# Kernel tuning notes

Hardware: AMD Instinct MI355X
Metric: run time of the kernel (lower is better)

## Reference

```python
import jax, jax.numpy as jnp
import numpy as np

H = 1024
N_HEADS = 8
HEAD_DIM = H // N_HEADS
META_DIM = 256
VOCAB = 32000
MIN_W, MAX_W = 0.1, 5.0
LN_EPS = 1e-5


def _ln(x, g, b):
    mu = jnp.mean(x, axis=-1, keepdims=True)
    var = jnp.var(x, axis=-1, keepdims=True)
    return (x - mu) * jax.lax.rsqrt(var + LN_EPS) * g + b


def setup_inputs() -> dict:
    key = jax.random.key(0)
    ks = jax.random.split(key, 16)
    B, S = 4, 2048
    s = 0.02
    return {
        "hidden_states": jax.random.normal(ks[0], (B, S, H), jnp.float32),
        "token_ids": jax.random.randint(ks[1], (B, S), 0, VOCAB, jnp.int32),
        "attention_mask": jnp.ones((B, S), jnp.bool_),
        "pos_embed": jax.random.normal(ks[2], (1, S, H), jnp.float32),
        # torch nn.MultiheadAttention params
        "in_proj_w": jax.random.normal(ks[3], (3 * H, H), jnp.float32) * s,
        "in_proj_b": jnp.zeros((3 * H,), jnp.float32),
        "out_w": jax.random.normal(ks[4], (H, H), jnp.float32) * s,
        "out_b": jnp.zeros((H,), jnp.float32),
        # meta_network params (torch Linear convention: y = x @ W.T + b)
        "w1": jax.random.normal(ks[5], (META_DIM, 2 * H), jnp.float32) * s,
        "b1": jnp.zeros((META_DIM,), jnp.float32),
        "g1": jnp.ones((META_DIM,), jnp.float32),
        "beta1": jnp.zeros((META_DIM,), jnp.float32),
        "w2": jax.random.normal(ks[6], (META_DIM // 2, META_DIM), jnp.float32) * s,
        "b2": jnp.zeros((META_DIM // 2,), jnp.float32),
        "g2": jnp.ones((META_DIM // 2,), jnp.float32),
        "beta2": jnp.zeros((META_DIM // 2,), jnp.float32),
        "w3": jax.random.normal(ks[7], (1, META_DIM // 2), jnp.float32) * s,
        "b3": jnp.zeros((1,), jnp.float32),
        # tensorized ImportanceMemory.get_importance: one scalar per vocab id
        "importance_table": jax.random.uniform(ks[8], (VOCAB,), jnp.float32) * 0.1,
    }


def reference(hidden_states, token_ids, attention_mask, pos_embed,
              in_proj_w, in_proj_b, out_w, out_b,
              w1, b1, g1, beta1, w2, b2, g2, beta2, w3, b3,
              importance_table):
    B, S, _ = hidden_states.shape
    x = hidden_states + pos_embed[:, :S, :]

    # MultiheadAttention (batch_first, eval mode -> no dropout)
    qkv = x @ in_proj_w.T + in_proj_b                      # [B,S,3H]
    q, k, v = jnp.split(qkv, 3, axis=-1)
    q = q.reshape(B, S, N_HEADS, HEAD_DIM)
    k = k.reshape(B, S, N_HEADS, HEAD_DIM)
    v = v.reshape(B, S, N_HEADS, HEAD_DIM)
    scores = jnp.einsum('bqhd,bkhd->bhqk', q, k) / jnp.sqrt(jnp.float32(HEAD_DIM))
    scores = jnp.where(attention_mask[:, None, None, :], scores, jnp.float32(-1e9))
    attn = jax.nn.softmax(scores, axis=-1)
    ctx = jnp.einsum('bhqk,bkhd->bqhd', attn, v).reshape(B, S, H)
    attended = ctx @ out_w.T + out_b

    combined = jnp.concatenate([x, attended], axis=-1)     # [B,S,2H]
    h = jax.nn.relu(_ln(combined @ w1.T + b1, g1, beta1))
    h = jax.nn.relu(_ln(h @ w2.T + b2, g2, beta2))
    base_weights = (h @ w3.T + b3).squeeze(-1)             # [B,S]

    # tensorized per-token importance lookup + clamp (manual_weights empty)
    importance = importance_table[token_ids]               # gather [B,S]
    weight = jnp.clip(base_weights * (1.0 + importance), MIN_W, MAX_W)
    return jnp.where(attention_mask, weight, 0.0)
```

## Files before the change

kernel.cpp:

```cpp
#include <hip/hip_runtime.h>
#include <hip/hip_bf16.h>
#include <math.h>

typedef __bf16 bf16;
typedef bf16 bf16x8 __attribute__((ext_vector_type(8)));
typedef bf16 bf16x4 __attribute__((ext_vector_type(4)));
typedef float f32x4 __attribute__((ext_vector_type(4)));

#define HDIM 1024
#define NHEADS 8
#define HD 128
#define MD1 256
#define MD2 128
#define LNEPS 1e-5f

__device__ __forceinline__ f32x4 mfma16(bf16x8 a, bf16x8 b, f32x4 c) {
  return __builtin_amdgcn_mfma_f32_16x16x32_bf16(a, b, c, 0, 0, 0);
}

__device__ __forceinline__ void gload_lds16(const bf16* g, bf16* l) {
  __builtin_amdgcn_global_load_lds(
      (const __attribute__((address_space(1))) void*)g,
      (__attribute__((address_space(3))) void*)l, 16, 0, 0);
}

__global__ void k_prep_all(
    const float* __restrict__ hs, const float* __restrict__ pos,
    bf16* __restrict__ xbf, int SH, int nprep,
    const float* __restrict__ s0, bf16* __restrict__ d0, int n0,
    const float* __restrict__ s1, bf16* __restrict__ d1, int n1,
    const float* __restrict__ s2, bf16* __restrict__ d2, int n2,
    const float* __restrict__ s3, bf16* __restrict__ d3, int n3) {
  int i = (blockIdx.x * blockDim.x + threadIdx.x) * 4;
  if (i < nprep) {
    float4 a = *(const float4*)(hs + i);
    float4 p = *(const float4*)(pos + (i % SH));
    bf16x4 o;
    o[0] = (bf16)(a.x + p.x); o[1] = (bf16)(a.y + p.y);
    o[2] = (bf16)(a.z + p.z); o[3] = (bf16)(a.w + p.w);
    *(bf16x4*)(xbf + i) = o;
    return;
  }
  int j = i - nprep;
  const float* s; bf16* d;
  if (j < n0)                { s = s0 + j; d = d0 + j; }
  else if (j < n0 + n1)      { s = s1 + (j - n0); d = d1 + (j - n0); }
  else if (j < n0 + n1 + n2) { s = s2 + (j - n0 - n1); d = d2 + (j - n0 - n1); }
  else                       { s = s3 + (j - n0 - n1 - n2); d = d3 + (j - n0 - n1 - n2); }
  float4 v = *(const float4*)s;
  bf16x4 o;
  o[0] = (bf16)v.x; o[1] = (bf16)v.y; o[2] = (bf16)v.z; o[3] = (bf16)v.w;
  *(bf16x4*)d = o;
}

__global__ void k_b1p(const float* __restrict__ w1, const float* __restrict__ ob,
                      const float* __restrict__ b1, float* __restrict__ b1p) {
  const int t = threadIdx.x;
  const int n = blockIdx.x * 64 + (t >> 2);
  const int jq = t & 3;
  const float* row = w1 + (size_t)n * 2048 + 1024 + jq * 256;
  const float* obp = ob + jq * 256;
  float acc = 0.f;
  for (int j = 0; j < 256; j += 4) {
    float4 a = *(const float4*)(row + j);
    float4 o = *(const float4*)(obp + j);
    acc += a.x * o.x + a.y * o.y + a.z * o.z + a.w * o.w;
  }
  acc += __shfl_xor(acc, 1);
  acc += __shfl_xor(acc, 2);
  if (jq == 0) b1p[n] = b1[n] + acc;
}

__global__ __launch_bounds__(256) void k_wprime(
    const bf16* __restrict__ w1full, const bf16* __restrict__ ow,
    bf16* __restrict__ Wp) {
  __shared__ bf16 Bst[64][40];
  const int tid = threadIdx.x;
  const int w = tid >> 6, lane = tid & 63;
  const int quad = lane >> 4, l16 = lane & 15;
  const int d0 = blockIdx.x * 64, n0 = blockIdx.y * 64;
  const bf16* arow = w1full + (size_t)(n0 + w * 16 + l16) * 2048 + 1024;
  f32x4 acc[4] = {};
  for (int k0 = 0; k0 < 1024; k0 += 32) {
    const int kk = tid >> 3, dd8 = (tid & 7) * 8;
    bf16x8 v = *(const bf16x8*)(ow + (size_t)(k0 + kk) * 1024 + d0 + dd8);
    __syncthreads();
#pragma unroll
    for (int jj = 0; jj < 8; ++jj) Bst[dd8 + jj][kk] = v[jj];
    __syncthreads();
    bf16x8 af = *(const bf16x8*)(arow + k0 + quad * 8);
#pragma unroll
    for (int dg = 0; dg < 4; ++dg) {
      bf16x8 bfr = *(const bf16x8*)&Bst[dg * 16 + l16][quad * 8];
      acc[dg] = mfma16(af, bfr, acc[dg]);
    }
  }
#pragma unroll
  for (int dg = 0; dg < 4; ++dg) {
    const int d = d0 + dg * 16 + l16;
#pragma unroll
    for (int i = 0; i < 4; ++i)
      Wp[(size_t)(n0 + w * 16 + quad * 4 + i) * 1024 + d] = (bf16)acc[dg][i];
  }
}

__global__ __launch_bounds__(256) void k_gemm_qkv(
    const bf16* __restrict__ A, const bf16* __restrict__ Bw,
    const float* __restrict__ bias, bf16* __restrict__ Qo,
    bf16* __restrict__ Ko, bf16* __restrict__ VTo, int S, int K) {
  __shared__ bf16 As[128 * 64];
  __shared__ bf16 Bs[128 * 64];
  const int tid = threadIdx.x;
  const int w = tid >> 6, lane = tid & 63;
  const int quad = lane >> 4, l16 = lane & 15;
  const int wm = w & 1, wn = w >> 1;
  const int tm = blockIdx.x * 128, tn = blockIdx.y * 128;

  const int tq = tid >> 3, t8 = tid & 7;
  const bf16 *ap[4], *bp[4];
#pragma unroll
  for (int c = 0; c < 4; ++c) {
    const int r = c * 32 + tq;
    const int col = ((t8 ^ ((r ^ (r >> 3)) & 7)) * 8);
    ap[c] = A + (size_t)(tm + r) * K + col;
    bp[c] = Bw + (size_t)(tn + r) * K + col;
  }
  bf16* lA = As + (size_t)tid * 8;
  bf16* lB = Bs + (size_t)tid * 8;

  int fam[4], fbn[4], ram[4], rbn[4];
#pragma unroll
  for (int mt = 0; mt < 4; ++mt) {
    const int r = wm * 64 + mt * 16 + l16;
    ram[mt] = r; fam[mt] = (r ^ (r >> 3)) & 7;
    const int r2 = wn * 64 + mt * 16 + l16;
    rbn[mt] = r2; fbn[mt] = (r2 ^ (r2 >> 3)) & 7;
  }

  f32x4 acc[4][4] = {};
  for (int k0 = 0; k0 < K; k0 += 64) {
#pragma unroll
    for (int c = 0; c < 4; ++c) {
      gload_lds16(ap[c] + k0, lA + c * 2048);
      gload_lds16(bp[c] + k0, lB + c * 2048);
    }
    __syncthreads();
#pragma unroll
    for (int ks = 0; ks < 2; ++ks) {
      bf16x8 af[4], bfr[4];
#pragma unroll
      for (int mt = 0; mt < 4; ++mt)
        af[mt] = *(const bf16x8*)&As[ram[mt] * 64 + (((ks * 4 + quad) ^ fam[mt]) << 3)];
#pragma unroll
      for (int nt = 0; nt < 4; ++nt)
        bfr[nt] = *(const bf16x8*)&Bs[rbn[nt] * 64 + (((ks * 4 + quad) ^ fbn[nt]) << 3)];
#pragma unroll
      for (int mt = 0; mt < 4; ++mt)
#pragma unroll
        for (int nt = 0; nt < 4; ++nt)
          acc[mt][nt] = mfma16(af[mt], bfr[nt], acc[mt][nt]);
    }
    __syncthreads();
  }

  const int region = tn >> 10;
  const int btile = tm / S, s0 = tm % S;
#pragma unroll
  for (int nt = 0; nt < 4; ++nt) {
    const int col = tn + wn * 64 + nt * 16 + l16;
    const float bv = bias[col];
#pragma unroll
    for (int mt = 0; mt < 4; ++mt) {
      if (region == 2) {
        const int d = col - 2048, hh = d >> 7, dd = d & 127;
        const int sb = s0 + wm * 64 + mt * 16 + quad * 4;
        bf16x4 o4;
#pragma unroll
        for (int i = 0; i < 4; ++i) o4[i] = (bf16)(acc[mt][nt][i] + bv);
        *(bf16x4*)&VTo[((size_t)(btile * NHEADS + hh) * HD + dd) * S + sb] = o4;
      } else {
        bf16* dst = (region == 0) ? Qo : Ko;
        const int cc = (region == 0) ? col : col - 1024;
#pragma unroll
        for (int i = 0; i < 4; ++i) {
          const int row = tm + wm * 64 + mt * 16 + quad * 4 + i;
          dst[(size_t)row * HDIM + cc] = (bf16)(acc[mt][nt][i] + bv);
        }
      }
    }
  }
}

__global__ __launch_bounds__(256) void k_flash(
    const bf16* __restrict__ Qg, const bf16* __restrict__ Kg,
    const bf16* __restrict__ VTg, const int* __restrict__ mask,
    bf16* __restrict__ ctx, int S) {
  __shared__ bf16 Ks[64][136];
  __shared__ bf16 Vt[128 * 64];
  __shared__ bf16 Ps[8 * 1024];
  __shared__ float biass[64];
  const int tid = threadIdx.x, w = tid >> 6, lane = tid & 63;
  const int quad = lane >> 4, l16 = lane & 15;
  const int bh = blockIdx.y, b = bh / NHEADS, h = bh % NHEADS;
  const int q0 = blockIdx.x * 128 + w * 32;
  const size_t bS = (size_t)b * S;
  const bf16* Qb = Qg + bS * HDIM + h * HD;
  const bf16* Kb = Kg + bS * HDIM + h * HD;
  const bf16* Vb = VTg + (size_t)bh * HD * S;
  const int* mrow = mask + bS;

  bf16x8 qf[2][4];
#pragma unroll
  for (int qt = 0; qt < 2; ++qt)
#pragma unroll
    for (int s = 0; s < 4; ++s)
      qf[qt][s] = *(const bf16x8*)(Qb + (size_t)(q0 + qt * 16 + l16) * HDIM + s * 32 + quad * 8);

  float lsum[2] = {0.f, 0.f};
  f32x4 o[2][8] = {};
  const float scale2 = 0.08838834764831845f * 1.4426950408889634f;

  const int nchunk = S / 64;
  bf16x8 kreg[4], vreg[4];
  int mreg = (tid < 64) ? mrow[tid] : 0;
#pragma unroll
  for (int it = 0; it < 4; ++it) {
    const int cid = tid + it * 256;
    kreg[it] = *(const bf16x8*)(Kb + (size_t)(cid >> 4) * HDIM + (cid & 15) * 8);
    vreg[it] = *(const bf16x8*)(Vb + (size_t)(cid >> 3) * S + (cid & 7) * 8);
  }

  for (int c0 = 0; c0 < nchunk; ++c0) {
    __syncthreads();
#pragma unroll
    for (int it = 0; it < 4; ++it) {
      const int cid = tid + it * 256;
      *(bf16x8*)&Ks[cid >> 4][(cid & 15) * 8] = kreg[it];
      const int vd = cid >> 3, vkb = cid & 7;
      *(bf16x8*)&Vt[vd * 64 + ((vkb ^ (vd & 7)) << 3)] = vreg[it];
    }
    if (tid < 64) biass[tid] = mreg ? 0.f : -1e9f;
    __syncthreads();
    const int key0n = ((c0 + 1 < nchunk) ? c0 + 1 : c0) * 64;
    if (tid < 64) mreg = mrow[key0n + tid];
#pragma unroll
    for (int it = 0; it < 4; ++it) {
      const int cid = tid + it * 256;
      kreg[it] = *(const bf16x8*)(Kb + (size_t)(key0n + (cid >> 4)) * HDIM + (cid & 15) * 8);
      vreg[it] = *(const bf16x8*)(Vb + (size_t)(cid >> 3) * S + key0n + (cid & 7) * 8);
    }
    f32x4 s4[2][4] = {};
#pragma unroll
    for (int g = 0; g < 4; ++g)
#pragma unroll
      for (int s = 0; s < 4; ++s) {
        bf16x8 kf = *(const bf16x8*)&Ks[g * 16 + l16][s * 32 + quad * 8];
        s4[0][g] = mfma16(kf, qf[0][s], s4[0][g]);
        s4[1][g] = mfma16(kf, qf[1][s], s4[1][g]);
      }
#pragma unroll
    for (int qt = 0; qt < 2; ++qt) {
      const int base = (w * 2 + qt) * 1024;
#pragma unroll
      for (int g = 0; g < 4; ++g) {
        bf16x4 pk;
#pragma unroll
        for (int i = 0; i < 4; ++i) {
          const float p = exp2f(fmaf(s4[qt][g][i], scale2, biass[g * 16 + quad * 4 + i]));
          lsum[qt] += p;
          pk[i] = (bf16)p;
        }
        const int sw = (2 * g + (quad >> 1)) ^ (l16 & 7);
        *(bf16x4*)&Ps[base + l16 * 64 + sw * 8 + (quad & 1) * 4] = pk;
      }
    }
#pragma unroll
    for (int kk = 0; kk < 2; ++kk) {
      const int kb = kk * 4 + quad;
      bf16x8 pf0 = *(const bf16x8*)&Ps[(w * 2) * 1024 + l16 * 64 + ((kb ^ (l16 & 7)) << 3)];
      bf16x8 pf1 = *(const bf16x8*)&Ps[(w * 2 + 1) * 1024 + l16 * 64 + ((kb ^ (l16 & 7)) << 3)];
#pragma unroll
      for (int dg = 0; dg < 8; ++dg) {
        const int d = dg * 16 + l16;
        bf16x8 vf = *(const bf16x8*)&Vt[d * 64 + ((kb ^ (d & 7)) << 3)];
        o[0][dg] = mfma16(pf0, vf, o[0][dg]);
        o[1][dg] = mfma16(pf1, vf, o[1][dg]);
      }
    }
  }

#pragma unroll
  for (int qt = 0; qt < 2; ++qt) {
    lsum[qt] += __shfl_xor(lsum[qt], 16);
    lsum[qt] += __shfl_xor(lsum[qt], 32);
  }
#pragma unroll
  for (int qt = 0; qt < 2; ++qt)
#pragma unroll
    for (int i = 0; i < 4; ++i) {
      const float ls = __shfl(lsum[qt], quad * 4 + i);
      const float inv = 1.0f / ls;
      const int row = q0 + qt * 16 + quad * 4 + i;
#pragma unroll
      for (int dg = 0; dg < 8; ++dg)
        ctx[(bS + row) * HDIM + h * HD + dg * 16 + l16] = (bf16)(o[qt][dg][i] * inv);
    }
}

__global__ __launch_bounds__(256) void k_meta12(
    const bf16* __restrict__ A1, const bf16* __restrict__ A2,
    const bf16* __restrict__ Bw1, const bf16* __restrict__ Wp,
    const float* __restrict__ b1p, const float* __restrict__ g1,
    const float* __restrict__ be1,
    const bf16* __restrict__ Bw2, const float* __restrict__ b2,
    const float* __restrict__ g2, const float* __restrict__ be2,
    const float* __restrict__ w3, const float* __restrict__ b3,
    const int* __restrict__ tok, const int* __restrict__ msk,
    const float* __restrict__ imp, float* __restrict__ out) {
  __shared__ char smem[44032];
  __shared__ float part_s[64][4];
  __shared__ float part_q[64][4];
  bf16 (*As)[40]  = (bf16(*)[40])smem;
  bf16 (*Bs)[40]  = (bf16(*)[40])(smem + 5120);
  bf16 (*h1s)[264] = (bf16(*)[264])smem;
  bf16 (*Bs2)[40] = (bf16(*)[40])(smem + 33792);
  const int tid = threadIdx.x;
  const int w = tid >> 6, lane = tid & 63;
  const int quad = lane >> 4, l16 = lane & 15;
  const int tm = blockIdx.x * 64;
  const int lr = tid >> 2, lc = (tid & 3) * 8;

  f32x4 acc[4][4] = {};
  for (int k0 = 0; k0 < 2048; k0 += 32) {
    const int kg = k0 + lc;
    const bf16* ap = (kg < 1024) ? (A1 + (size_t)(tm + lr) * 1024 + kg)
                                 : (A2 + (size_t)(tm + lr) * 1024 + (kg - 1024));
    *(bf16x8*)&As[lr][lc] = *(const bf16x8*)ap;
#pragma unroll
    for (int it = 0; it < 4; ++it) {
      const int row = lr + it * 64;
      const bf16* bp = (kg < 1024) ? (Bw1 + (size_t)row * 2048 + kg)
                                   : (Wp + (size_t)row * 1024 + (kg - 1024));
      *(bf16x8*)&Bs[row][lc] = *(const bf16x8*)bp;
    }
    __syncthreads();
    bf16x8 af[4], bfr[4];
#pragma unroll
    for (int mt = 0; mt < 4; ++mt) af[mt] = *(const bf16x8*)&As[mt * 16 + l16][quad * 8];
#pragma unroll
    for (int nt = 0; nt < 4; ++nt)
      bfr[nt] = *(const bf16x8*)&Bs[w * 64 + nt * 16 + l16][quad * 8];
#pragma unroll
    for (int mt = 0; mt < 4; ++mt)
#pragma unroll
      for (int nt = 0; nt < 4; ++nt)
        acc[mt][nt] = mfma16(af[mt], bfr[nt], acc[mt][nt]);
    __syncthreads();
  }

  float bv[4], gv[4], bev[4];
#pragma unroll
  for (int nt = 0; nt < 4; ++nt) {
    const int col = w * 64 + nt * 16 + l16;
    bv[nt] = b1p[col]; gv[nt] = g1[col]; bev[nt] = be1[col];
  }
#pragma unroll
  for (int mt = 0; mt < 4; ++mt)
#pragma unroll
    for (int i = 0; i < 4; ++i) {
      float s = 0.f, q = 0.f;
#pragma unroll
      for (int nt = 0; nt < 4; ++nt) {
        const float v = acc[mt][nt][i] + bv[nt];
        s += v; q += v * v;
      }
#pragma unroll
      for (int off = 1; off < 16; off <<= 1) { s += __shfl_xor(s, off); q += __shfl_xor(q, off); }
      if (l16 == 0) {
        const int row = mt * 16 + quad * 4 + i;
        part_s[row][w] = s; part_q[row][w] = q;
      }
    }
  __syncthreads();
#pragma unroll
  for (int mt = 0; mt < 4; ++mt)
#pragma unroll
    for (int i = 0; i < 4; ++i) {
      const int row = mt * 16 + quad * 4 + i;
      const float4 ps = *(const float4*)part_s[row];
      const float4 pq = *(const float4*)part_q[row];
      const float sum = ps.x + ps.y + ps.z + ps.w;
      const float sq = pq.x + pq.y + pq.z + pq.w;
      const float mean = sum / MD1;
      const float var = sq / MD1 - mean * mean;
      const float r = rsqrtf(var + LNEPS);
#pragma unroll
      for (int nt = 0; nt < 4; ++nt) {
        const int col = w * 64 + nt * 16 + l16;
        const float v = acc[mt][nt][i] + bv[nt];
        const float t = (v - mean) * r * gv[nt] + bev[nt];
        h1s[row][col] = (bf16)fmaxf(t, 0.f);
      }
    }
  __syncthreads();

  f32x4 acc2[8] = {};
  for (int k0 = 0; k0 < MD1; k0 += 32) {
    const int kg = k0 + lc;
#pragma unroll
    for (int it = 0; it < 2; ++it)
      *(bf16x8*)&Bs2[lr + it * 64][lc] =
          *(const bf16x8*)(Bw2 + (size_t)(lr + it * 64) * MD1 + kg);
    __syncthreads();
    bf16x8 af = *(const bf16x8*)&h1s[w * 16 + l16][k0 + quad * 8];
#pragma unroll
    for (int nt = 0; nt < 8; ++nt) {
      bf16x8 bfr = *(const bf16x8*)&Bs2[nt * 16 + l16][quad * 8];
      acc2[nt] = mfma16(af, bfr, acc2[nt]);
    }
    __syncthreads();
  }

  float bv2[8], gv2[8], bev2[8], w3v[8];
#pragma unroll
  for (int nt = 0; nt < 8; ++nt) {
    const int col = nt * 16 + l16;
    bv2[nt] = b2[col]; gv2[nt] = g2[col]; bev2[nt] = be2[col]; w3v[nt] = w3[col];
  }
  const float b3v = b3[0];
#pragma unroll
  for (int i = 0; i < 4; ++i) {
    float s = 0.f, q = 0.f;
#pragma unroll
    for (int nt = 0; nt < 8; ++nt) {
      const float v = acc2[nt][i] + bv2[nt];
      s += v; q += v * v;
    }
#pragma unroll
    for (int off = 1; off < 16; off <<= 1) { s += __shfl_xor(s, off); q += __shfl_xor(q, off); }
    const float mean = s / MD2;
    const float var = q / MD2 - mean * mean;
    const float r = rsqrtf(var + LNEPS);
    float d = 0.f;
#pragma unroll
    for (int nt = 0; nt < 8; ++nt) {
      const float v = acc2[nt][i] + bv2[nt];
      const float t = (v - mean) * r * gv2[nt] + bev2[nt];
      d += fmaxf(t, 0.f) * w3v[nt];
    }
#pragma unroll
    for (int off = 1; off < 16; off <<= 1) d += __shfl_xor(d, off);
    if (l16 == 0) {
      const int row = tm + w * 16 + quad * 4 + i;
      float wt = (d + b3v) * (1.f + imp[tok[row]]);
      wt = fminf(fmaxf(wt, 0.1f), 5.0f);
      out[row] = msk[row] ? wt : 0.f;
    }
  }
}

extern "C" void kernel_launch(void* const* d_in, const int* in_sizes, int n_in,
                              void* d_out, int out_size, void* d_ws, size_t ws_size,
                              hipStream_t stream) {
  const float* hs  = (const float*)d_in[0];
  const int*   tok = (const int*)d_in[1];
  const int*   msk = (const int*)d_in[2];
  const float* pos = (const float*)d_in[3];
  const float* inw = (const float*)d_in[4];
  const float* inb = (const float*)d_in[5];
  const float* ow  = (const float*)d_in[6];
  const float* ob  = (const float*)d_in[7];
  const float* w1  = (const float*)d_in[8];
  const float* b1  = (const float*)d_in[9];
  const float* g1  = (const float*)d_in[10];
  const float* be1 = (const float*)d_in[11];
  const float* w2  = (const float*)d_in[12];
  const float* b2  = (const float*)d_in[13];
  const float* g2  = (const float*)d_in[14];
  const float* be2 = (const float*)d_in[15];
  const float* w3  = (const float*)d_in[16];
  const float* b3  = (const float*)d_in[17];
  const float* imp = (const float*)d_in[18];

  const int SH = in_sizes[3];
  const int S  = SH / HDIM;
  const int Bsz = in_sizes[0] / SH;
  const int M = Bsz * S;

  char* ws = (char*)d_ws;
  const size_t MB2 = (size_t)M * HDIM * 2;
  size_t off = 0;
  bf16* xbf = (bf16*)(ws + off);  off += MB2;
  bf16* Qb  = (bf16*)(ws + off);  off += MB2;
  bf16* Kb  = (bf16*)(ws + off);  off += MB2;
  bf16* VTb = (bf16*)(ws + off);  off += MB2;
  bf16* ctx = (bf16*)(ws + off);  off += MB2;
  bf16* winp = (bf16*)(ws + off); off += (size_t)3 * HDIM * HDIM * 2;
  bf16* wout = (bf16*)(ws + off); off += (size_t)HDIM * HDIM * 2;
  bf16* w1b = (bf16*)(ws + off);  off += (size_t)MD1 * 2 * HDIM * 2;
  bf16* w2b = (bf16*)(ws + off);  off += (size_t)MD2 * MD1 * 2;
  bf16* Wp  = (bf16*)(ws + off);  off += (size_t)MD1 * HDIM * 2;
  float* b1p = (float*)(ws + off); off += (size_t)MD1 * 4;

  const int nprep = M * HDIM;
  const int n0 = 3 * HDIM * HDIM, n1 = HDIM * HDIM, n2 = MD1 * 2 * HDIM, n3 = MD2 * MD1;
  k_prep_all<<<(nprep + n0 + n1 + n2 + n3) / 4 / 256, 256, 0, stream>>>(
      hs, pos, xbf, SH, nprep, inw, winp, n0, ow, wout, n1, w1, w1b, n2, w2, w2b, n3);
  k_b1p<<<MD1 / 64, 256, 0, stream>>>(w1, ob, b1, b1p);
  k_wprime<<<dim3(HDIM / 64, MD1 / 64), 256, 0, stream>>>(w1b, wout, Wp);
  k_gemm_qkv<<<dim3(M / 128, (3 * HDIM) / 128), 256, 0, stream>>>(
      xbf, winp, inb, Qb, Kb, VTb, S, HDIM);
  k_flash<<<dim3(S / 128, Bsz * NHEADS), 256, 0, stream>>>(Qb, Kb, VTb, msk, ctx, S);
  k_meta12<<<M / 64, 256, 0, stream>>>(xbf, ctx, w1b, Wp, b1p, g1, be1,
                                       w2b, b2, g2, be2, w3, b3, tok, msk, imp,
                                       (float*)d_out);
}
```

Baseline: 382.7 us.

## Fuse weight-prep kernels and switch flash attention to direct global-to-LDS loads

Merges the conversion, W' product and bias-fold kernels into one launch by block-index dispatch. The W' product now reads fp32 weights directly, so the bf16 out-projection copy is no longer written. The flash kernel now loads K and V tiles with global_load_lds into XOR-swizzled LDS instead of staging them through registers, and remaps the 1-D grid so blocks that share a head run near each other. This lowers launch count and register pressure, but the prefetch overlap is lost because loads are issued and waited on within the same iteration, and the grid remap hardcodes the shape (8 heads × 4 batches, 16 q-blocks).

```diff
diff --git a/kernel.cpp b/kernel.cpp
--- a/kernel.cpp
+++ b/kernel.cpp
@@ -24,42 +24,82 @@
       (__attribute__((address_space(3))) void*)l, 16, 0, 0);
 }
 
-__global__ void k_prep_all(
+__global__ __launch_bounds__(256) void k_prep_all(
     const float* __restrict__ hs, const float* __restrict__ pos,
     bf16* __restrict__ xbf, int SH, int nprep,
-    const float* __restrict__ s0, bf16* __restrict__ d0, int n0,
-    const float* __restrict__ s1, bf16* __restrict__ d1, int n1,
-    const float* __restrict__ s2, bf16* __restrict__ d2, int n2,
-    const float* __restrict__ s3, bf16* __restrict__ d3, int n3) {
-  int i = (blockIdx.x * blockDim.x + threadIdx.x) * 4;
-  if (i < nprep) {
-    float4 a = *(const float4*)(hs + i);
-    float4 p = *(const float4*)(pos + (i % SH));
+    const float* __restrict__ inwf, bf16* __restrict__ winp, int n0,
+    const float* __restrict__ w1f, bf16* __restrict__ w1b, int n2,
+    const float* __restrict__ w2f, bf16* __restrict__ w2b, int n3,
+    const float* __restrict__ owf, const float* __restrict__ obf,
+    const float* __restrict__ b1f, bf16* __restrict__ Wp,
+    float* __restrict__ b1p, int blocks_el) {
+  const int bid = blockIdx.x;
+  const int tid = threadIdx.x;
+  if (bid < blocks_el) {
+    int i = (bid * 256 + tid) * 4;
+    if (i < nprep) {
+      float4 a = *(const float4*)(hs + i);
+      float4 p = *(const float4*)(pos + (i % SH));
+      bf16x4 o;
+      o[0] = (bf16)(a.x + p.x); o[1] = (bf16)(a.y + p.y);
+      o[2] = (bf16)(a.z + p.z); o[3] = (bf16)(a.w + p.w);
+      *(bf16x4*)(xbf + i) = o;
+      return;
+    }
+    int j = i - nprep;
+    const float* s; bf16* d;
+    if (j < n0)           { s = inwf + j; d = winp + j; }
+    else if (j < n0 + n2) { s = w1f + (j - n0); d = w1b + (j - n0); }
+    else                  { s = w2f + (j - n0 - n2); d = w2b + (j - n0 - n2); }
+    float4 v = *(const float4*)s;
     bf16x4 o;
-    o[0] = (bf16)(a.x + p.x); o[1] = (bf16)(a.y + p.y);
-    o[2] = (bf16)(a.z + p.z); o[3] = (bf16)(a.w + p.w);
-    *(bf16x4*)(xbf + i) = o;
+    o[0] = (bf16)v.x; o[1] = (bf16)v.y; o[2] = (bf16)v.z; o[3] = (bf16)v.w;
+    *(bf16x4*)d = o;
     return;
   }
-  int j = i - nprep;
-  const float* s; bf16* d;
-  if (j < n0)                { s = s0 + j; d = d0 + j; }
-  else if (j < n0 + n1)      { s = s1 + (j - n0); d = d1 + (j - n0); }
-  else if (j < n0 + n1 + n2) { s = s2 + (j - n0 - n1); d = d2 + (j - n0 - n1); }
-  else                       { s = s3 + (j - n0 - n1 - n2); d = d3 + (j - n0 - n1 - n2); }
-  float4 v = *(const float4*)s;
-  bf16x4 o;
-  o[0] = (bf16)v.x; o[1] = (bf16)v.y; o[2] = (bf16)v.z; o[3] = (bf16)v.w;
-  *(bf16x4*)d = o;
-}
-
-__global__ void k_b1p(const float* __restrict__ w1, const float* __restrict__ ob,
-                      const float* __restrict__ b1, float* __restrict__ b1p) {
-  const int t = threadIdx.x;
-  const int n = blockIdx.x * 64 + (t >> 2);
-  const int jq = t & 3;
-  const float* row = w1 + (size_t)n * 2048 + 1024 + jq * 256;
-  const float* obp = ob + jq * 256;
+  if (bid < blocks_el + 64) {
+    __shared__ bf16 Bst[64][42];
+    const int bid2 = bid - blocks_el;
+    const int d0 = (bid2 & 15) * 64, n0w = (bid2 >> 4) * 64;
+    const int w = tid >> 6, lane = tid & 63;
+    const int quad = lane >> 4, l16 = lane & 15;
+    const float* arow = w1f + (size_t)(n0w + w * 16 + l16) * 2048 + 1024;
+    f32x4 acc[4] = {};
+    for (int k0 = 0; k0 < 1024; k0 += 32) {
+      const int kk = tid >> 3, dd8 = (tid & 7) * 8;
+      float4 va = *(const float4*)(owf + (size_t)(k0 + kk) * 1024 + d0 + dd8);
+      float4 vb = *(const float4*)(owf + (size_t)(k0 + kk) * 1024 + d0 + dd8 + 4);
+      __syncthreads();
+      Bst[dd8 + 0][kk] = (bf16)va.x; Bst[dd8 + 1][kk] = (bf16)va.y;
+      Bst[dd8 + 2][kk] = (bf16)va.z; Bst[dd8 + 3][kk] = (bf16)va.w;
+      Bst[dd8 + 4][kk] = (bf16)vb.x; Bst[dd8 + 5][kk] = (bf16)vb.y;
+      Bst[dd8 + 6][kk] = (bf16)vb.z; Bst[dd8 + 7][kk] = (bf16)vb.w;
+      __syncthreads();
+      float4 fa = *(const float4*)(arow + k0 + quad * 8);
+      float4 fb = *(const float4*)(arow + k0 + quad * 8 + 4);
+      bf16x8 af;
+      af[0] = (bf16)fa.x; af[1] = (bf16)fa.y; af[2] = (bf16)fa.z; af[3] = (bf16)fa.w;
+      af[4] = (bf16)fb.x; af[5] = (bf16)fb.y; af[6] = (bf16)fb.z; af[7] = (bf16)fb.w;
+#pragma unroll
+      for (int dg = 0; dg < 4; ++dg) {
+        bf16x8 bfr = *(const bf16x8*)&Bst[dg * 16 + l16][quad * 8];
+        acc[dg] = mfma16(af, bfr, acc[dg]);
+      }
+    }
+#pragma unroll
+    for (int dg = 0; dg < 4; ++dg) {
+      const int d = d0 + dg * 16 + l16;
+#pragma unroll
+      for (int i = 0; i < 4; ++i)
+        Wp[(size_t)(n0w + w * 16 + quad * 4 + i) * 1024 + d] = (bf16)acc[dg][i];
+    }
+    return;
+  }
+  const int bid3 = bid - blocks_el - 64;
+  const int n = bid3 * 64 + (tid >> 2);
+  const int jq = tid & 3;
+  const float* row = w1f + (size_t)n * 2048 + 1024 + jq * 256;
+  const float* obp = obf + jq * 256;
   float acc = 0.f;
   for (int j = 0; j < 256; j += 4) {
     float4 a = *(const float4*)(row + j);
@@ -68,40 +108,7 @@
   }
   acc += __shfl_xor(acc, 1);
   acc += __shfl_xor(acc, 2);
-  if (jq == 0) b1p[n] = b1[n] + acc;
-}
-
-__global__ __launch_bounds__(256) void k_wprime(
-    const bf16* __restrict__ w1full, const bf16* __restrict__ ow,
-    bf16* __restrict__ Wp) {
-  __shared__ bf16 Bst[64][40];
-  const int tid = threadIdx.x;
-  const int w = tid >> 6, lane = tid & 63;
-  const int quad = lane >> 4, l16 = lane & 15;
-  const int d0 = blockIdx.x * 64, n0 = blockIdx.y * 64;
-  const bf16* arow = w1full + (size_t)(n0 + w * 16 + l16) * 2048 + 1024;
-  f32x4 acc[4] = {};
-  for (int k0 = 0; k0 < 1024; k0 += 32) {
-    const int kk = tid >> 3, dd8 = (tid & 7) * 8;
-    bf16x8 v = *(const bf16x8*)(ow + (size_t)(k0 + kk) * 1024 + d0 + dd8);
-    __syncthreads();
-#pragma unroll
-    for (int jj = 0; jj < 8; ++jj) Bst[dd8 + jj][kk] = v[jj];
-    __syncthreads();
-    bf16x8 af = *(const bf16x8*)(arow + k0 + quad * 8);
-#pragma unroll
-    for (int dg = 0; dg < 4; ++dg) {
-      bf16x8 bfr = *(const bf16x8*)&Bst[dg * 16 + l16][quad * 8];
-      acc[dg] = mfma16(af, bfr, acc[dg]);
-    }
-  }
-#pragma unroll
-  for (int dg = 0; dg < 4; ++dg) {
-    const int d = d0 + dg * 16 + l16;
-#pragma unroll
-    for (int i = 0; i < 4; ++i)
-      Wp[(size_t)(n0 + w * 16 + quad * 4 + i) * 1024 + d] = (bf16)acc[dg][i];
-  }
+  if (jq == 0) b1p[n] = b1f[n] + acc;
 }
 
 __global__ __launch_bounds__(256) void k_gemm_qkv(
@@ -195,20 +202,36 @@
     const bf16* __restrict__ Qg, const bf16* __restrict__ Kg,
     const bf16* __restrict__ VTg, const int* __restrict__ mask,
     bf16* __restrict__ ctx, int S) {
-  __shared__ bf16 Ks[64][136];
+  __shared__ bf16 Ks[64 * 128];
   __shared__ bf16 Vt[128 * 64];
   __shared__ bf16 Ps[8 * 1024];
   __shared__ float biass[64];
   const int tid = threadIdx.x, w = tid >> 6, lane = tid & 63;
   const int quad = lane >> 4, l16 = lane & 15;
-  const int bh = blockIdx.y, b = bh / NHEADS, h = bh % NHEADS;
-  const int q0 = blockIdx.x * 128 + w * 32;
+  const int p = blockIdx.x;
+  const int bh = (p & 7) * 4 + ((p >> 3) >> 4);
+  const int qb = (p >> 3) & 15;
+  const int b = bh / NHEADS, h = bh % NHEADS;
+  const int q0 = qb * 128 + w * 32;
   const size_t bS = (size_t)b * S;
   const bf16* Qb = Qg + bS * HDIM + h * HD;
   const bf16* Kb = Kg + bS * HDIM + h * HD;
   const bf16* Vb = VTg + (size_t)bh * HD * S;
   const int* mrow = mask + bS;
 
+  const bf16 *ksrc[4], *vsrc[4];
+#pragma unroll
+  for (int it = 0; it < 4; ++it) {
+    const int key = it * 16 + (tid >> 4);
+    const int g = tid & 15;
+    const int fk = (key ^ (key >> 3)) & 7;
+    const int db = (g & 8) | ((g ^ fk) & 7);
+    ksrc[it] = Kb + (size_t)key * HDIM + db * 8;
+    const int d = it * 32 + (tid >> 3);
+    const int kb = (tid & 7) ^ (d & 7);
+    vsrc[it] = Vb + (size_t)d * S + kb * 8;
+  }
+
   bf16x8 qf[2][4];
 #pragma unroll
   for (int qt = 0; qt < 2; ++qt)
@@ -219,45 +242,34 @@
   float lsum[2] = {0.f, 0.f};
   f32x4 o[2][8] = {};
   const float scale2 = 0.08838834764831845f * 1.4426950408889634f;
-
   const int nchunk = S / 64;
-  bf16x8 kreg[4], vreg[4];
-  int mreg = (tid < 64) ? mrow[tid] : 0;
-#pragma unroll
-  for (int it = 0; it < 4; ++it) {
-    const int cid = tid + it * 256;
-    kreg[it] = *(const bf16x8*)(Kb + (size_t)(cid >> 4) * HDIM + (cid & 15) * 8);
-    vreg[it] = *(const bf16x8*)(Vb + (size_t)(cid >> 3) * S + (cid & 7) * 8);
-  }
 
   for (int c0 = 0; c0 < nchunk; ++c0) {
     __syncthreads();
 #pragma unroll
     for (int it = 0; it < 4; ++it) {
-      const int cid = tid + it * 256;
-      *(bf16x8*)&Ks[cid >> 4][(cid & 15) * 8] = kreg[it];
-      const int vd = cid >> 3, vkb = cid & 7;
-      *(bf16x8*)&Vt[vd * 64 + ((vkb ^ (vd & 7)) << 3)] = vreg[it];
-    }
-    if (tid < 64) biass[tid] = mreg ? 0.f : -1e9f;
-    __syncthreads();
-    const int key0n = ((c0 + 1 < nchunk) ? c0 + 1 : c0) * 64;
-    if (tid < 64) mreg = mrow[key0n + tid];
-#pragma unroll
-    for (int it = 0; it < 4; ++it) {
-      const int cid = tid + it * 256;
-      kreg[it] = *(const bf16x8*)(Kb + (size_t)(key0n + (cid >> 4)) * HDIM + (cid & 15) * 8);
-      vreg[it] = *(const bf16x8*)(Vb + (size_t)(cid >> 3) * S + key0n + (cid & 7) * 8);
-    }
+      gload_lds16(ksrc[it], Ks + it * 2048 + tid * 8);
+      gload_lds16(vsrc[it], Vt + it * 2048 + tid * 8);
+      ksrc[it] += 64 * HDIM;
+      vsrc[it] += 64;
+    }
+    if (tid < 64) biass[tid] = mrow[c0 * 64 + tid] ? 0.f : -1e9f;
+    __syncthreads();
+
     f32x4 s4[2][4] = {};
 #pragma unroll
-    for (int g = 0; g < 4; ++g)
+    for (int g = 0; g < 4; ++g) {
+      const int key = g * 16 + l16;
+      const int fk = (key ^ (key >> 3)) & 7;
 #pragma unroll
       for (int s = 0; s < 4; ++s) {
-        bf16x8 kf = *(const bf16x8*)&Ks[g * 16 + l16][s * 32 + quad * 8];
+        const int db = s * 4 + quad;
+        const int gr = (db & 8) | ((db ^ fk) & 7);
+        bf16x8 kf = *(const bf16x8*)&Ks[key * 128 + gr * 8];
         s4[0][g] = mfma16(kf, qf[0][s], s4[0][g]);
         s4[1][g] = mfma16(kf, qf[1][s], s4[1][g]);
       }
+    }
 #pragma unroll
     for (int qt = 0; qt < 2; ++qt) {
       const int base = (w * 2 + qt) * 1024;
@@ -266,9 +278,9 @@
         bf16x4 pk;
 #pragma unroll
         for (int i = 0; i < 4; ++i) {
-          const float p = exp2f(fmaf(s4[qt][g][i], scale2, biass[g * 16 + quad * 4 + i]));
-          lsum[qt] += p;
-          pk[i] = (bf16)p;
+          const float pv = exp2f(fmaf(s4[qt][g][i], scale2, biass[g * 16 + quad * 4 + i]));
+          lsum[qt] += pv;
+          pk[i] = (bf16)pv;
         }
         const int sw = (2 * g + (quad >> 1)) ^ (l16 & 7);
         *(bf16x4*)&Ps[base + l16 * 64 + sw * 8 + (quad & 1) * 4] = pk;
@@ -496,21 +508,20 @@
   bf16* VTb = (bf16*)(ws + off);  off += MB2;
   bf16* ctx = (bf16*)(ws + off);  off += MB2;
   bf16* winp = (bf16*)(ws + off); off += (size_t)3 * HDIM * HDIM * 2;
-  bf16* wout = (bf16*)(ws + off); off += (size_t)HDIM * HDIM * 2;
   bf16* w1b = (bf16*)(ws + off);  off += (size_t)MD1 * 2 * HDIM * 2;
   bf16* w2b = (bf16*)(ws + off);  off += (size_t)MD2 * MD1 * 2;
   bf16* Wp  = (bf16*)(ws + off);  off += (size_t)MD1 * HDIM * 2;
   float* b1p = (float*)(ws + off); off += (size_t)MD1 * 4;
 
   const int nprep = M * HDIM;
-  const int n0 = 3 * HDIM * HDIM, n1 = HDIM * HDIM, n2 = MD1 * 2 * HDIM, n3 = MD2 * MD1;
-  k_prep_all<<<(nprep + n0 + n1 + n2 + n3) / 4 / 256, 256, 0, stream>>>(
-      hs, pos, xbf, SH, nprep, inw, winp, n0, ow, wout, n1, w1, w1b, n2, w2, w2b, n3);
-  k_b1p<<<MD1 / 64, 256, 0, stream>>>(w1, ob, b1, b1p);
-  k_wprime<<<dim3(HDIM / 64, MD1 / 64), 256, 0, stream>>>(w1b, wout, Wp);
+  const int n0 = 3 * HDIM * HDIM, n2 = MD1 * 2 * HDIM, n3 = MD2 * MD1;
+  const int blocks_el = (nprep + n0 + n2 + n3) / 4 / 256;
+  k_prep_all<<<blocks_el + 64 + MD1 / 64, 256, 0, stream>>>(
+      hs, pos, xbf, SH, nprep, inw, winp, n0, w1, w1b, n2, w2, w2b, n3,
+      ow, ob, b1, Wp, b1p, blocks_el);
   k_gemm_qkv<<<dim3(M / 128, (3 * HDIM) / 128), 256, 0, stream>>>(
       xbf, winp, inb, Qb, Kb, VTb, S, HDIM);
-  k_flash<<<dim3(S / 128, Bsz * NHEADS), 256, 0, stream>>>(Qb, Kb, VTb, msk, ctx, S);
+  k_flash<<<(S / 128) * Bsz * NHEADS, 256, 0, stream>>>(Qb, Kb, VTb, msk, ctx, S);
   k_meta12<<<M / 64, 256, 0, stream>>>(xbf, ctx, w1b, Wp, b1p, g1, be1,
                                        w2b, b2, g2, be2, w3, b3, tok, msk, imp,
                                        (float*)d_out);
```

Result: faster. 372.3 us (-2.7%).
